# Kernel optimization log

Hardware: AMD Instinct MI355X
Metric: run time of the kernel (lower is better)

Reference implementation:

```python
import jax, jax.numpy as jnp
import numpy as np

B, T, D = 2, 1024, 1024
NUM_HEADS_ARG = 16
HS = D // NUM_HEADS_ARG          # 64 (per-head size)
H = HS                           # bug in source: num_heads passed = head_size -> 64 heads
FF = 4 * D
EPS = 1e-5


def _layernorm(x, gamma, beta):
    mu = jnp.mean(x, axis=-1, keepdims=True)
    var = jnp.mean(jnp.square(x - mu), axis=-1, keepdims=True)
    return (x - mu) * jax.lax.rsqrt(var + EPS) * gamma + beta


def setup_inputs() -> dict:
    key = jax.random.key(0)
    ks = jax.random.split(key, 12)
    s_d = 1.0 / np.sqrt(D)
    s_cat = 1.0 / np.sqrt(H * HS)
    s_ff = 1.0 / np.sqrt(FF)
    return {
        "x": jax.random.normal(ks[0], (B, T, D), jnp.float32),
        "Wq": jax.random.uniform(ks[1], (H, D, HS), jnp.float32, -s_d, s_d),
        "Wk": jax.random.uniform(ks[2], (H, D, HS), jnp.float32, -s_d, s_d),
        "Wv": jax.random.uniform(ks[3], (H, D, HS), jnp.float32, -s_d, s_d),
        "Wo": jax.random.uniform(ks[4], (H * HS, D), jnp.float32, -s_cat, s_cat),
        "bo": jax.random.uniform(ks[5], (D,), jnp.float32, -s_cat, s_cat),
        "W1": jax.random.uniform(ks[6], (D, FF), jnp.float32, -s_d, s_d),
        "b1": jax.random.uniform(ks[7], (FF,), jnp.float32, -s_d, s_d),
        "W2": jax.random.uniform(ks[8], (FF, D), jnp.float32, -s_ff, s_ff),
        "b2": jax.random.uniform(ks[9], (D,), jnp.float32, -s_ff, s_ff),
        "g1": jnp.ones((D,), jnp.float32),
        "be1": jnp.zeros((D,), jnp.float32),
        "g2": jnp.ones((D,), jnp.float32),
        "be2": jnp.zeros((D,), jnp.float32),
    }


def reference(x, Wq, Wk, Wv, Wo, bo, W1, b1, W2, b2, g1, be1, g2, be2):
    # per-head projections (no bias): [B,H,T,hs]
    q = jnp.einsum('btd,hde->bhte', x, Wq)
    k = jnp.einsum('btd,hde->bhte', x, Wk)
    v = jnp.einsum('btd,hde->bhte', x, Wv)
    scores = jnp.einsum('bhte,bhse->bhts', q, k) / np.sqrt(HS)  # [B,H,T,T]
    causal = jnp.tril(jnp.ones((T, T), bool))
    scores = jnp.where(causal, scores, -jnp.inf)
    probs = jax.nn.softmax(scores, axis=-1)
    att = jnp.einsum('bhts,bhse->bhte', probs, v)               # [B,H,T,hs]
    # torch stack(dim=3) -> [B,T,hs,H] then flatten: index = d*H + h
    cat = jnp.transpose(att, (0, 2, 3, 1)).reshape(B, T, HS * H)
    mha = cat @ Wo + bo
    x1 = _layernorm(x + mha, g1, be1)
    ff = jax.nn.relu(x1 @ W1 + b1) @ W2 + b2
    return _layernorm(x1 + ff, g2, be2)
```

## Files before the change

### kernel.cpp

```cpp
#include <hip/hip_runtime.h>

typedef unsigned short u16;
typedef __bf16 bf16x8 __attribute__((ext_vector_type(8)));
typedef float f32x4 __attribute__((ext_vector_type(4)));

#define B_ 2
#define T_ 1024
#define D_ 1024
#define H_ 64
#define HS_ 64
#define FF_ 4096
#define SZ_QKV 8388608L
#define S_SCALE 0.1803368801111f

__device__ __forceinline__ float bf2f(u16 u) {
  union { unsigned int v; float f; } x; x.v = ((unsigned int)u) << 16; return x.f;
}
__device__ __forceinline__ u16 f2bf(float f) {
  union { float f; unsigned int v; } x; x.f = f;
  unsigned int r = x.v + 0x7fffu + ((x.v >> 16) & 1u);
  return (u16)(r >> 16);
}
__device__ __forceinline__ u16 f2bf_rtz(float f) {
  union { float f; unsigned int v; } x; x.f = f;
  return (u16)(x.v >> 16);
}

typedef __attribute__((address_space(3))) unsigned int lds_u32;
typedef __attribute__((address_space(1))) const unsigned int glb_u32;
__device__ __forceinline__ void gload_lds16(const void* g, void* l) {
  __builtin_amdgcn_global_load_lds((glb_u32*)g, (lds_u32*)l, 16, 0, 0);
}

__global__ __launch_bounds__(256) void prep(
    const float* __restrict__ x, const float* __restrict__ Wq,
    const float* __restrict__ Wk, const float* __restrict__ Wv,
    const float* __restrict__ Wo, const float* __restrict__ W1,
    const float* __restrict__ W2,
    u16* __restrict__ xb, u16* __restrict__ Wqkvt, u16* __restrict__ Wot,
    u16* __restrict__ W1t, u16* __restrict__ W2t)
{
  __shared__ float tile[64][65];
  int id = blockIdx.x;
  if (id < 1024) {
    const long i = ((long)id * 256 + threadIdx.x) * 8;
    float4 a = *(const float4*)(x + i);
    float4 b = *(const float4*)(x + i + 4);
    union { uint4 v; u16 u[8]; } o;
    o.u[0]=f2bf(a.x); o.u[1]=f2bf(a.y); o.u[2]=f2bf(a.z); o.u[3]=f2bf(a.w);
    o.u[4]=f2bf(b.x); o.u[5]=f2bf(b.y); o.u[6]=f2bf(b.z); o.u[7]=f2bf(b.w);
    *(uint4*)(xb + i) = o.v;
    return;
  }
  id -= 1024;
  const float* in; u16* out; long ibase, obase; int in_rs, out_rs, r0, c0;
  if (id < 3072) {
    const int w = id >> 10, rem = id & 1023;
    const int z = rem >> 4, rt = rem & 15;
    in = (w == 0) ? Wq : (w == 1) ? Wk : Wv;
    ibase = (long)z * 65536; in_rs = 64; r0 = rt * 64; c0 = 0;
    out = Wqkvt + (long)w * 4194304;
    obase = (long)z * 65536; out_rs = 1024;
  } else if (id < 4096) {
    const int rem = id - 3072;
    const int z = rem >> 4, ct = rem & 15;
    in = Wo; ibase = (long)z * 1024; in_rs = 65536; r0 = 0; c0 = ct * 64;
    out = Wot; obase = (long)z * 64; out_rs = 4096;
  } else if (id < 5120) {
    const int rem = id - 4096;
    const int rt = rem >> 6, ct = rem & 63;
    in = W1; ibase = 0; in_rs = 4096; r0 = rt * 64; c0 = ct * 64;
    out = W1t; obase = 0; out_rs = 1024;
  } else {
    const int rem = id - 5120;
    const int rt = rem >> 4, ct = rem & 15;
    in = W2; ibase = 0; in_rs = 1024; r0 = rt * 64; c0 = ct * 64;
    out = W2t; obase = 0; out_rs = 4096;
  }
  const int t = threadIdx.x, lr = t >> 4, lc4 = (t & 15) * 4;
  #pragma unroll
  for (int j = 0; j < 4; ++j) {
    float4 f = *(const float4*)(in + ibase + (long)(r0 + lr + j * 16) * in_rs + c0 + lc4);
    tile[lr + j * 16][lc4]     = f.x;
    tile[lr + j * 16][lc4 + 1] = f.y;
    tile[lr + j * 16][lc4 + 2] = f.z;
    tile[lr + j * 16][lc4 + 3] = f.w;
  }
  __syncthreads();
  const int cr = t >> 3, ch = t & 7;
  #pragma unroll
  for (int j2 = 0; j2 < 2; ++j2) {
    const int crr = cr + j2 * 32;
    union { uint4 v; u16 u[8]; } o;
    #pragma unroll
    for (int i = 0; i < 8; ++i) o.u[i] = f2bf(tile[ch * 8 + i][crr]);
    *(uint4*)(out + obase + (long)(c0 + crr) * out_rs + r0 + ch * 8) = o.v;
  }
}

template<int EPI, int LDA, int LDB>
__global__ __launch_bounds__(512, 2) void gemm8b(
    const u16* __restrict__ A, const u16* __restrict__ Bt, u16* __restrict__ C,
    const float* __restrict__ bias, int K, int koff, int ldc)
{
  __shared__ __attribute__((aligned(16))) u16 As[3][256 * 64];
  __shared__ __attribute__((aligned(16))) u16 Bs[3][128 * 64];
  const int nwg = gridDim.x, cpx = nwg >> 3;
  const int sid = (blockIdx.x & 7) * cpx + (blockIdx.x >> 3);
  const int bm = sid & 7, bn = sid >> 3;
  const int bz = blockIdx.z;
  const long ko = (long)bz * koff;
  const int tid = threadIdx.x, wave = tid >> 6, lane = tid & 63;
  const int quad = lane >> 4, l16 = lane & 15;
  const int wm = (wave >> 1) * 64;
  const int wn = (wave & 1) * 64;
  const int slog = ((tid & 7) ^ ((tid >> 3) & 7)) * 8;
  const int srow = tid >> 3;
  const int ph0 = ((quad)     ^ (l16 & 7)) * 8;
  const int ph1 = ((4 + quad) ^ (l16 & 7)) * 8;

  const u16* Ag = A + (long)(bm * 256) * LDA + ko + slog;
  const u16* Bg = Bt + (long)(bn * 128) * LDB + ko + slog;

  f32x4 acc[4][4];
  #pragma unroll
  for (int i = 0; i < 4; ++i)
    #pragma unroll
    for (int j = 0; j < 4; ++j) acc[i][j] = (f32x4){0.f, 0.f, 0.f, 0.f};

  const int nK = K >> 6;

  auto STAGE_A = [&](int d, int t, int a) {
    gload_lds16(Ag + (long)(a * 64 + srow) * LDA + (t << 6),
                (u16*)As[d] + a * 4096 + tid * 8);
  };
  auto STAGE_B = [&](int d, int t, int b) {
    gload_lds16(Bg + (long)(b * 64 + srow) * LDB + (t << 6),
                (u16*)Bs[d] + b * 4096 + tid * 8);
  };

  #pragma unroll
  for (int a = 0; a < 4; ++a) STAGE_A(0, 0, a);
  STAGE_B(0, 0, 0); STAGE_B(0, 0, 1);
  #pragma unroll
  for (int a = 0; a < 4; ++a) STAGE_A(1, 1, a);
  STAGE_B(1, 1, 0); STAGE_B(1, 1, 1);

  bf16x8 af[4][2], bf[4][2];
  int cur = 0;
  for (int t = 0; t < nK; ++t) {
    const int nxt = (cur >= 1) ? cur - 1 : cur + 2;
    const bool st = (t + 2) < nK;
    const u16* Ab = As[cur];
    const u16* Bb = Bs[cur];

    if (t < nK - 1) { asm volatile("s_waitcnt vmcnt(6)" ::: "memory"); }
    else            { asm volatile("s_waitcnt vmcnt(0)" ::: "memory"); }
    __builtin_amdgcn_sched_barrier(0);
    __builtin_amdgcn_s_barrier();
    __builtin_amdgcn_sched_barrier(0);

    #pragma unroll
    for (int ii = 0; ii < 2; ++ii) {
      const u16* r = Ab + (wm + ii * 16 + l16) * 64;
      af[ii][0] = *(const bf16x8*)(r + ph0);
      af[ii][1] = *(const bf16x8*)(r + ph1);
    }
    #pragma unroll
    for (int jj = 0; jj < 2; ++jj) {
      const u16* r = Bb + (wn + jj * 16 + l16) * 64;
      bf[jj][0] = *(const bf16x8*)(r + ph0);
      bf[jj][1] = *(const bf16x8*)(r + ph1);
    }
    if (st) { STAGE_A(nxt, t + 2, 0); STAGE_A(nxt, t + 2, 1); }
    __builtin_amdgcn_sched_barrier(0);
    __builtin_amdgcn_s_setprio(1);
    #pragma unroll
    for (int ii = 0; ii < 2; ++ii)
      #pragma unroll
      for (int jj = 0; jj < 2; ++jj) {
        acc[ii][jj] = __builtin_amdgcn_mfma_f32_16x16x32_bf16(af[ii][0], bf[jj][0], acc[ii][jj], 0, 0, 0);
        acc[ii][jj] = __builtin_amdgcn_mfma_f32_16x16x32_bf16(af[ii][1], bf[jj][1], acc[ii][jj], 0, 0, 0);
      }
    __builtin_amdgcn_s_setprio(0);
    __builtin_amdgcn_sched_barrier(0);

    #pragma unroll
    for (int jj = 0; jj < 2; ++jj) {
      const u16* r = Bb + (wn + (2 + jj) * 16 + l16) * 64;
      bf[2 + jj][0] = *(const bf16x8*)(r + ph0);
      bf[2 + jj][1] = *(const bf16x8*)(r + ph1);
    }
    if (st) { STAGE_A(nxt, t + 2, 2); STAGE_A(nxt, t + 2, 3); }
    __builtin_amdgcn_sched_barrier(0);
    __builtin_amdgcn_s_setprio(1);
    #pragma unroll
    for (int ii = 0; ii < 2; ++ii)
      #pragma unroll
      for (int jj = 0; jj < 2; ++jj) {
        acc[ii][2 + jj] = __builtin_amdgcn_mfma_f32_16x16x32_bf16(af[ii][0], bf[2 + jj][0], acc[ii][2 + jj], 0, 0, 0);
        acc[ii][2 + jj] = __builtin_amdgcn_mfma_f32_16x16x32_bf16(af[ii][1], bf[2 + jj][1], acc[ii][2 + jj], 0, 0, 0);
      }
    __builtin_amdgcn_s_setprio(0);
    __builtin_amdgcn_sched_barrier(0);

    #pragma unroll
    for (int ii = 0; ii < 2; ++ii) {
      const u16* r = Ab + (wm + (2 + ii) * 16 + l16) * 64;
      af[2 + ii][0] = *(const bf16x8*)(r + ph0);
      af[2 + ii][1] = *(const bf16x8*)(r + ph1);
    }
    if (st) { STAGE_B(nxt, t + 2, 0); STAGE_B(nxt, t + 2, 1); }
    __builtin_amdgcn_sched_barrier(0);
    __builtin_amdgcn_s_setprio(1);
    #pragma unroll
    for (int ii = 0; ii < 2; ++ii)
      #pragma unroll
      for (int jj = 0; jj < 2; ++jj) {
        acc[2 + ii][jj] = __builtin_amdgcn_mfma_f32_16x16x32_bf16(af[2 + ii][0], bf[jj][0], acc[2 + ii][jj], 0, 0, 0);
        acc[2 + ii][jj] = __builtin_amdgcn_mfma_f32_16x16x32_bf16(af[2 + ii][1], bf[jj][1], acc[2 + ii][jj], 0, 0, 0);
      }
    __builtin_amdgcn_s_setprio(0);
    __builtin_amdgcn_sched_barrier(0);

    __builtin_amdgcn_s_setprio(1);
    #pragma unroll
    for (int ii = 0; ii < 2; ++ii)
      #pragma unroll
      for (int jj = 0; jj < 2; ++jj) {
        acc[2 + ii][2 + jj] = __builtin_amdgcn_mfma_f32_16x16x32_bf16(af[2 + ii][0], bf[2 + jj][0], acc[2 + ii][2 + jj], 0, 0, 0);
        acc[2 + ii][2 + jj] = __builtin_amdgcn_mfma_f32_16x16x32_bf16(af[2 + ii][1], bf[2 + jj][1], acc[2 + ii][2 + jj], 0, 0, 0);
      }
    __builtin_amdgcn_s_setprio(0);

    cur = nxt == 0 ? (cur == 2 ? 0 : cur + 1) : (cur == 2 ? 0 : cur + 1);
  }

  #pragma unroll
  for (int j = 0; j < 4; ++j) {
    const int col = bn * 128 + wn + j * 16 + l16;
    const float bval = (EPI == 1) ? bias[col] : 0.f;
    #pragma unroll
    for (int i = 0; i < 4; ++i) {
      #pragma unroll
      for (int r = 0; r < 4; ++r) {
        const int row = bm * 256 + wm + i * 16 + quad * 4 + r;
        float vv = acc[i][j][r] + bval;
        if (EPI == 1) vv = fmaxf(vv, 0.f);
        if (EPI == 2) {
          const int which = col >> 12, rem = col & 4095;
          const int h = rem >> 6, e = rem & 63;
          const int bb = row >> 10, tt = row & 1023;
          C[(long)which * SZ_QKV + ((long)((bb << 6) + h)) * 65536L + tt * 64 + e] = f2bf(vv);
        } else if (EPI == 3) {
          ((float*)C)[(long)bz * 2097152 + (long)row * ldc + col] = vv;
        } else {
          C[(long)row * ldc + col] = f2bf(vv);
        }
      }
    }
  }
}

__global__ __launch_bounds__(256) void attn_flash(
    const u16* __restrict__ Q, const u16* __restrict__ Kg,
    const u16* __restrict__ V, u16* __restrict__ Om)
{
  __shared__ __attribute__((aligned(16))) u16 Ks[2][64][72];
  __shared__ __attribute__((aligned(16))) u16 Vs[2][64][72];
  __shared__ __attribute__((aligned(16))) u16 QP[4][16][72];
  const int bh = blockIdx.x;
  const int qt = gridDim.y - 1 - blockIdx.y;
  const int b = bh >> 6, h = bh & 63;
  const long base = (long)bh * (T_ * HS_);
  const int tid = threadIdx.x;
  const int wave = tid >> 6, lane = tid & 63, quad = lane >> 4, l16 = lane & 15;
  const int sm = tid >> 2, sc = (tid & 3) * 16;
  const int vswz = (sc >> 4) << 3;

  {
    const int qr = lane >> 3, qe = (lane & 7) * 8;
    #pragma unroll
    for (int j = 0; j < 2; ++j) {
      union { uint4 v; u16 u[8]; } a, o;
      a.v = *(const uint4*)(Q + base + (long)(qt * 64 + wave * 16 + qr + j * 8) * HS_ + qe);
      #pragma unroll
      for (int i = 0; i < 8; ++i) o.u[i] = f2bf(bf2f(a.u[i]) * S_SCALE);
      *(uint4*)&QP[wave][qr + j * 8][qe] = o.v;
    }
  }
  bf16x8 aq0 = *(const bf16x8*)&QP[wave][l16][quad * 8];
  bf16x8 aq1 = *(const bf16x8*)&QP[wave][l16][32 + quad * 8];

  float psum[4] = { 0.f, 0.f, 0.f, 0.f };
  f32x4 oacc[4] = { {0,0,0,0}, {0,0,0,0}, {0,0,0,0}, {0,0,0,0} };

  uint4 kA, kB, vA, vB;
  kA = *(const uint4*)(Kg + base + (long)sm * HS_ + sc);
  kB = *(const uint4*)(Kg + base + (long)sm * HS_ + sc + 8);
  vA = *(const uint4*)(V  + base + (long)sm * HS_ + sc);
  vB = *(const uint4*)(V  + base + (long)sm * HS_ + sc + 8);
  {
    *(uint4*)&Ks[0][sm][sc] = kA; *(uint4*)&Ks[0][sm][sc + 8] = kB;
    union { uint4 v; u16 u[8]; } t0, t1; t0.v = vA; t1.v = vB;
    #pragma unroll
    for (int i = 0; i < 8; ++i) Vs[0][sc + i][sm ^ vswz] = t0.u[i];
    #pragma unroll
    for (int i = 0; i < 8; ++i) Vs[0][sc + 8 + i][sm ^ vswz] = t1.u[i];
  }
  __syncthreads();

  for (int kt = 0; kt <= qt; ++kt) {
    const int cur = kt & 1;
    const bool pf = (kt < qt);
    if (pf) {
      const long nb = base + (long)((kt + 1) * 64 + sm) * HS_ + sc;
      kA = *(const uint4*)(Kg + nb); kB = *(const uint4*)(Kg + nb + 8);
      vA = *(const uint4*)(V  + nb); vB = *(const uint4*)(V  + nb + 8);
    }

    f32x4 sacc[4] = { {0,0,0,0}, {0,0,0,0}, {0,0,0,0}, {0,0,0,0} };
    #pragma unroll
    for (int nt = 0; nt < 4; ++nt) {
      bf16x8 b0 = *(const bf16x8*)&Ks[cur][nt * 16 + l16][quad * 8];
      bf16x8 b1 = *(const bf16x8*)&Ks[cur][nt * 16 + l16][32 + quad * 8];
      sacc[nt] = __builtin_amdgcn_mfma_f32_16x16x32_bf16(aq0, b0, sacc[nt], 0, 0, 0);
      sacc[nt] = __builtin_amdgcn_mfma_f32_16x16x32_bf16(aq1, b1, sacc[nt], 0, 0, 0);
    }

    if (kt == qt) {
      #pragma unroll
      for (int nt = 0; nt < 4; ++nt) {
        const int col = nt * 16 + l16;
        #pragma unroll
        for (int r = 0; r < 4; ++r) {
          const int row = wave * 16 + quad * 4 + r;
          float p = exp2f(sacc[nt][r]);
          p = (col <= row) ? p : 0.f;
          sacc[nt][r] = p; psum[r] += p;
        }
      }
    } else {
      #pragma unroll
      for (int nt = 0; nt < 4; ++nt)
        #pragma unroll
        for (int r = 0; r < 4; ++r) {
          const float p = exp2f(sacc[nt][r]);
          sacc[nt][r] = p; psum[r] += p;
        }
    }

    #pragma unroll
    for (int nt = 0; nt < 4; ++nt)
      #pragma unroll
      for (int r = 0; r < 4; ++r)
        QP[wave][quad * 4 + r][nt * 16 + l16] = f2bf_rtz(sacc[nt][r]);
    bf16x8 p0 = *(const bf16x8*)&QP[wave][l16][quad * 8];
    bf16x8 p1 = *(const bf16x8*)&QP[wave][l16][32 + quad * 8];

    #pragma unroll
    for (int et = 0; et < 4; ++et) {
      const int c0 = ((quad ^ et) * 8);
      bf16x8 b0 = *(const bf16x8*)&Vs[cur][et * 16 + l16][c0];
      bf16x8 b1 = *(const bf16x8*)&Vs[cur][et * 16 + l16][32 + c0];
      oacc[et] = __builtin_amdgcn_mfma_f32_16x16x32_bf16(p0, b0, oacc[et], 0, 0, 0);
      oacc[et] = __builtin_amdgcn_mfma_f32_16x16x32_bf16(p1, b1, oacc[et], 0, 0, 0);
    }

    if (pf) {
      const int nxt = 1 - cur;
      *(uint4*)&Ks[nxt][sm][sc] = kA; *(uint4*)&Ks[nxt][sm][sc + 8] = kB;
      union { uint4 v; u16 u[8]; } t0, t1; t0.v = vA; t1.v = vB;
      #pragma unroll
      for (int i = 0; i < 8; ++i) Vs[nxt][sc + i][sm ^ vswz] = t0.u[i];
      #pragma unroll
      for (int i = 0; i < 8; ++i) Vs[nxt][sc + 8 + i][sm ^ vswz] = t1.u[i];
    }
    __syncthreads();
  }

  #pragma unroll
  for (int off = 1; off < 16; off <<= 1)
    #pragma unroll
    for (int r = 0; r < 4; ++r)
      psum[r] += __shfl_xor(psum[r], off, 64);
  u16 (*Os)[72] = Ks[0];
  #pragma unroll
  for (int r = 0; r < 4; ++r) {
    const float rinv = 1.f / fmaxf(psum[r], 1e-20f);
    const int row = wave * 16 + quad * 4 + r;
    #pragma unroll
    for (int et = 0; et < 4; ++et)
      Os[row][et * 16 + l16] = f2bf(oacc[et][r] * rinv);
  }
  const int orow = wave * 16 + (lane >> 3), oe = (lane & 7) * 8;
  #pragma unroll
  for (int it = 0; it < 2; ++it) {
    const int rr = orow + it * 8;
    uint4 o = *(const uint4*)&Os[rr][oe];
    *(uint4*)(Om + ((long)(b * T_ + qt * 64 + rr)) * 4096 + h * 64 + oe) = o;
  }
}

template<int XBF, int OBF>
__global__ __launch_bounds__(256) void ln_sum4(
    const float* __restrict__ P4, const float* __restrict__ bias,
    const void* __restrict__ Xv, const float* __restrict__ g,
    const float* __restrict__ be, void* __restrict__ outv)
{
  __shared__ float red[8];
  const int row = blockIdx.x, tid = threadIdx.x;
  const long base = (long)row * D_;
  float v4[4]; float s = 0.f;
  #pragma unroll
  for (int j = 0; j < 4; ++j) {
    const int i = tid + j * 256;
    float acc = bias[i];
    #pragma unroll
    for (int p = 0; p < 4; ++p) acc += P4[(long)p * 2097152 + base + i];
    const float xval = XBF ? bf2f(((const u16*)Xv)[base + i]) : ((const float*)Xv)[base + i];
    v4[j] = xval + acc;
    s += v4[j];
  }
  #pragma unroll
  for (int off = 32; off > 0; off >>= 1) s += __shfl_down(s, off, 64);
  if ((tid & 63) == 0) red[tid >> 6] = s;
  __syncthreads();
  const float mu = (red[0] + red[1] + red[2] + red[3]) * (1.f / D_);
  float vs = 0.f;
  #pragma unroll
  for (int j = 0; j < 4; ++j) { const float d = v4[j] - mu; vs += d * d; }
  #pragma unroll
  for (int off = 32; off > 0; off >>= 1) vs += __shfl_down(vs, off, 64);
  __syncthreads();
  if ((tid & 63) == 0) red[tid >> 6] = vs;
  __syncthreads();
  const float rs = rsqrtf((red[0] + red[1] + red[2] + red[3]) * (1.f / D_) + 1e-5f);
  #pragma unroll
  for (int j = 0; j < 4; ++j) {
    const int i = tid + j * 256;
    const float o = (v4[j] - mu) * rs * g[i] + be[i];
    if (OBF) ((u16*)outv)[base + i] = f2bf(o);
    else     ((float*)outv)[base + i] = o;
  }
}

extern "C" void kernel_launch(void* const* d_in, const int* in_sizes, int n_in,
                              void* d_out, int out_size, void* d_ws, size_t ws_size,
                              hipStream_t stream) {
  const float* x   = (const float*)d_in[0];
  const float* Wq  = (const float*)d_in[1];
  const float* Wk  = (const float*)d_in[2];
  const float* Wv  = (const float*)d_in[3];
  const float* Wo  = (const float*)d_in[4];
  const float* bo  = (const float*)d_in[5];
  const float* W1  = (const float*)d_in[6];
  const float* b1  = (const float*)d_in[7];
  const float* W2  = (const float*)d_in[8];
  const float* b2  = (const float*)d_in[9];
  const float* g1  = (const float*)d_in[10];
  const float* be1 = (const float*)d_in[11];
  const float* g2  = (const float*)d_in[12];
  const float* be2 = (const float*)d_in[13];
  float* out = (float*)d_out;

  u16* ws = (u16*)d_ws;
  u16* xb    = ws;
  u16* Wqkvt = xb + 2097152;
  u16* Wot   = Wqkvt + 12582912;
  u16* W1t   = Wot + 4194304;
  u16* W2t   = W1t + 4194304;
  u16* q     = W2t + 4194304;
  u16* k     = q + SZ_QKV;
  u16* v     = k + SZ_QKV;
  u16* Om    = v + SZ_QKV;
  float* P1 = (float*)q;
  float* P2 = (float*)q;
  u16* x1  = v;
  u16* h1  = Om;

  dim3 blk(256);
  dim3 blk8(512);

  prep<<<dim3(7168), blk, 0, stream>>>(x, Wq, Wk, Wv, Wo, W1, W2,
                                       xb, Wqkvt, Wot, W1t, W2t);

  gemm8b<2, 1024, 1024><<<dim3(768), blk8, 0, stream>>>(
      xb, Wqkvt, q, nullptr, 1024, 0, 0);

  attn_flash<<<dim3(128, 16), blk, 0, stream>>>(q, k, v, Om);

  gemm8b<3, 4096, 4096><<<dim3(64, 1, 4), blk8, 0, stream>>>(
      Om, Wot, (u16*)P1, nullptr, 1024, 1024, 1024);

  ln_sum4<0, 1><<<dim3(2048), blk, 0, stream>>>(P1, bo, x, g1, be1, x1);

  gemm8b<1, 1024, 1024><<<dim3(256), blk8, 0, stream>>>(
      x1, W1t, h1, b1, 1024, 0, 4096);

  gemm8b<3, 4096, 4096><<<dim3(64, 1, 4), blk8, 0, stream>>>(
      h1, W2t, (u16*)P2, nullptr, 1024, 1024, 1024);

  ln_sum4<1, 0><<<dim3(2048), blk, 0, stream>>>(P2, b2, x1, g2, be2, out);

  (void)in_sizes; (void)n_in; (void)out_size; (void)ws_size;
}
```

Baseline: 357.5 us.

## Switch GEMM to 4-wave blocks with K=32 steps and larger per-wave tiles

Replaces the 8-wave 256x128 GEMM with a 4-wave version. Each wave now computes a 128x64 sub-tile with 8x4 accumulators, and the K step per stage drops from 64 to 32, with a new LDS layout and swizzle that packs two rows per 64-element line. Fewer waves mean less barrier overhead, more register-level reuse of A/B fragments, and half the LDS footprint per block. The cost is higher accumulator register pressure, which may limit occupancy, plus twice as many loop iterations and barriers per K.

```diff
diff --git a/kernel.cpp b/kernel.cpp
--- a/kernel.cpp
+++ b/kernel.cpp
@@ -99,12 +99,12 @@
 }
 
 template<int EPI, int LDA, int LDB>
-__global__ __launch_bounds__(512, 2) void gemm8b(
+__global__ __launch_bounds__(256, 2) void gemm4w(
     const u16* __restrict__ A, const u16* __restrict__ Bt, u16* __restrict__ C,
     const float* __restrict__ bias, int K, int koff, int ldc)
 {
-  __shared__ __attribute__((aligned(16))) u16 As[3][256 * 64];
-  __shared__ __attribute__((aligned(16))) u16 Bs[3][128 * 64];
+  __shared__ __attribute__((aligned(16))) u16 As[3][8192];
+  __shared__ __attribute__((aligned(16))) u16 Bs[3][4096];
   const int nwg = gridDim.x, cpx = nwg >> 3;
   const int sid = (blockIdx.x & 7) * cpx + (blockIdx.x >> 3);
   const int bm = sid & 7, bn = sid >> 3;
@@ -112,31 +112,33 @@
   const long ko = (long)bz * koff;
   const int tid = threadIdx.x, wave = tid >> 6, lane = tid & 63;
   const int quad = lane >> 4, l16 = lane & 15;
-  const int wm = (wave >> 1) * 64;
+  const int wm = (wave >> 1) * 128;
   const int wn = (wave & 1) * 64;
-  const int slog = ((tid & 7) ^ ((tid >> 3) & 7)) * 8;
-  const int srow = tid >> 3;
-  const int ph0 = ((quad)     ^ (l16 & 7)) * 8;
-  const int ph1 = ((4 + quad) ^ (l16 & 7)) * 8;
-
-  const u16* Ag = A + (long)(bm * 256) * LDA + ko + slog;
-  const u16* Bg = Bt + (long)(bn * 128) * LDB + ko + slog;
-
-  f32x4 acc[4][4];
-  #pragma unroll
-  for (int i = 0; i < 4; ++i)
+
+  const int u_ = (tid & 7) ^ ((tid >> 3) & 7);
+  const int srow = 2 * (tid >> 3) + (u_ >> 2);
+  const int scol = (u_ & 3) * 8;
+  const int sA = ((((l16 & 1) << 2) + quad) ^ (l16 >> 1)) * 8;
+  const int Lb = l16 >> 1;
+
+  const u16* Ag = A + (long)(bm * 256 + srow) * LDA + ko + scol;
+  const u16* Bg = Bt + (long)(bn * 128 + srow) * LDB + ko + scol;
+
+  f32x4 acc[8][4];
+  #pragma unroll
+  for (int i = 0; i < 8; ++i)
     #pragma unroll
     for (int j = 0; j < 4; ++j) acc[i][j] = (f32x4){0.f, 0.f, 0.f, 0.f};
 
-  const int nK = K >> 6;
+  const int nK = K >> 5;
 
   auto STAGE_A = [&](int d, int t, int a) {
-    gload_lds16(Ag + (long)(a * 64 + srow) * LDA + (t << 6),
-                (u16*)As[d] + a * 4096 + tid * 8);
+    gload_lds16(Ag + (long)(a * 64) * LDA + (t << 5),
+                (u16*)As[d] + a * 2048 + tid * 8);
   };
   auto STAGE_B = [&](int d, int t, int b) {
-    gload_lds16(Bg + (long)(b * 64 + srow) * LDB + (t << 6),
-                (u16*)Bs[d] + b * 4096 + tid * 8);
+    gload_lds16(Bg + (long)(b * 64) * LDB + (t << 5),
+                (u16*)Bs[d] + b * 2048 + tid * 8);
   };
 
   #pragma unroll
@@ -146,10 +148,10 @@
   for (int a = 0; a < 4; ++a) STAGE_A(1, 1, a);
   STAGE_B(1, 1, 0); STAGE_B(1, 1, 1);
 
-  bf16x8 af[4][2], bf[4][2];
+  bf16x8 af[8], bf[4];
   int cur = 0;
   for (int t = 0; t < nK; ++t) {
-    const int nxt = (cur >= 1) ? cur - 1 : cur + 2;
+    const int nxt = (cur >= 1) ? cur - 1 : 2;
     const bool st = (t + 2) < nK;
     const u16* Ab = As[cur];
     const u16* Bb = Bs[cur];
@@ -161,79 +163,59 @@
     __builtin_amdgcn_sched_barrier(0);
 
     #pragma unroll
-    for (int ii = 0; ii < 2; ++ii) {
-      const u16* r = Ab + (wm + ii * 16 + l16) * 64;
-      af[ii][0] = *(const bf16x8*)(r + ph0);
-      af[ii][1] = *(const bf16x8*)(r + ph1);
-    }
-    #pragma unroll
-    for (int jj = 0; jj < 2; ++jj) {
-      const u16* r = Bb + (wn + jj * 16 + l16) * 64;
-      bf[jj][0] = *(const bf16x8*)(r + ph0);
-      bf[jj][1] = *(const bf16x8*)(r + ph1);
-    }
+    for (int i = 0; i < 4; ++i)
+      af[i] = *(const bf16x8*)&Ab[((wm >> 1) + i * 8 + Lb) * 64 + sA];
+    #pragma unroll
+    for (int j = 0; j < 2; ++j)
+      bf[j] = *(const bf16x8*)&Bb[((wn >> 1) + j * 8 + Lb) * 64 + sA];
     if (st) { STAGE_A(nxt, t + 2, 0); STAGE_A(nxt, t + 2, 1); }
     __builtin_amdgcn_sched_barrier(0);
     __builtin_amdgcn_s_setprio(1);
     #pragma unroll
-    for (int ii = 0; ii < 2; ++ii)
-      #pragma unroll
-      for (int jj = 0; jj < 2; ++jj) {
-        acc[ii][jj] = __builtin_amdgcn_mfma_f32_16x16x32_bf16(af[ii][0], bf[jj][0], acc[ii][jj], 0, 0, 0);
-        acc[ii][jj] = __builtin_amdgcn_mfma_f32_16x16x32_bf16(af[ii][1], bf[jj][1], acc[ii][jj], 0, 0, 0);
-      }
+    for (int i = 0; i < 4; ++i)
+      #pragma unroll
+      for (int j = 0; j < 2; ++j)
+        acc[i][j] = __builtin_amdgcn_mfma_f32_16x16x32_bf16(af[i], bf[j], acc[i][j], 0, 0, 0);
     __builtin_amdgcn_s_setprio(0);
     __builtin_amdgcn_sched_barrier(0);
 
     #pragma unroll
-    for (int jj = 0; jj < 2; ++jj) {
-      const u16* r = Bb + (wn + (2 + jj) * 16 + l16) * 64;
-      bf[2 + jj][0] = *(const bf16x8*)(r + ph0);
-      bf[2 + jj][1] = *(const bf16x8*)(r + ph1);
-    }
+    for (int j = 0; j < 2; ++j)
+      bf[2 + j] = *(const bf16x8*)&Bb[((wn >> 1) + (2 + j) * 8 + Lb) * 64 + sA];
     if (st) { STAGE_A(nxt, t + 2, 2); STAGE_A(nxt, t + 2, 3); }
     __builtin_amdgcn_sched_barrier(0);
     __builtin_amdgcn_s_setprio(1);
     #pragma unroll
-    for (int ii = 0; ii < 2; ++ii)
-      #pragma unroll
-      for (int jj = 0; jj < 2; ++jj) {
-        acc[ii][2 + jj] = __builtin_amdgcn_mfma_f32_16x16x32_bf16(af[ii][0], bf[2 + jj][0], acc[ii][2 + jj], 0, 0, 0);
-        acc[ii][2 + jj] = __builtin_amdgcn_mfma_f32_16x16x32_bf16(af[ii][1], bf[2 + jj][1], acc[ii][2 + jj], 0, 0, 0);
-      }
+    for (int i = 0; i < 4; ++i)
+      #pragma unroll
+      for (int j = 0; j < 2; ++j)
+        acc[i][2 + j] = __builtin_amdgcn_mfma_f32_16x16x32_bf16(af[i], bf[2 + j], acc[i][2 + j], 0, 0, 0);
     __builtin_amdgcn_s_setprio(0);
     __builtin_amdgcn_sched_barrier(0);
 
     #pragma unroll
-    for (int ii = 0; ii < 2; ++ii) {
-      const u16* r = Ab + (wm + (2 + ii) * 16 + l16) * 64;
-      af[2 + ii][0] = *(const bf16x8*)(r + ph0);
-      af[2 + ii][1] = *(const bf16x8*)(r + ph1);
-    }
+    for (int i = 0; i < 4; ++i)
+      af[4 + i] = *(const bf16x8*)&Ab[((wm >> 1) + (4 + i) * 8 + Lb) * 64 + sA];
     if (st) { STAGE_B(nxt, t + 2, 0); STAGE_B(nxt, t + 2, 1); }
     __builtin_amdgcn_sched_barrier(0);
     __builtin_amdgcn_s_setprio(1);
     #pragma unroll
-    for (int ii = 0; ii < 2; ++ii)
-      #pragma unroll
-      for (int jj = 0; jj < 2; ++jj) {
-        acc[2 + ii][jj] = __builtin_amdgcn_mfma_f32_16x16x32_bf16(af[2 + ii][0], bf[jj][0], acc[2 + ii][jj], 0, 0, 0);
-        acc[2 + ii][jj] = __builtin_amdgcn_mfma_f32_16x16x32_bf16(af[2 + ii][1], bf[jj][1], acc[2 + ii][jj], 0, 0, 0);
-      }
+    for (int i = 0; i < 4; ++i)
+      #pragma unroll
+      for (int j = 0; j < 2; ++j)
+        acc[4 + i][j] = __builtin_amdgcn_mfma_f32_16x16x32_bf16(af[4 + i], bf[j], acc[4 + i][j], 0, 0, 0);
     __builtin_amdgcn_s_setprio(0);
     __builtin_amdgcn_sched_barrier(0);
 
     __builtin_amdgcn_s_setprio(1);
     #pragma unroll
-    for (int ii = 0; ii < 2; ++ii)
-      #pragma unroll
-      for (int jj = 0; jj < 2; ++jj) {
-        acc[2 + ii][2 + jj] = __builtin_amdgcn_mfma_f32_16x16x32_bf16(af[2 + ii][0], bf[2 + jj][0], acc[2 + ii][2 + jj], 0, 0, 0);
-        acc[2 + ii][2 + jj] = __builtin_amdgcn_mfma_f32_16x16x32_bf16(af[2 + ii][1], bf[2 + jj][1], acc[2 + ii][2 + jj], 0, 0, 0);
-      }
+    for (int i = 0; i < 4; ++i)
+      #pragma unroll
+      for (int j = 0; j < 2; ++j)
+        acc[4 + i][2 + j] = __builtin_amdgcn_mfma_f32_16x16x32_bf16(af[4 + i], bf[2 + j], acc[4 + i][2 + j], 0, 0, 0);
     __builtin_amdgcn_s_setprio(0);
 
-    cur = nxt == 0 ? (cur == 2 ? 0 : cur + 1) : (cur == 2 ? 0 : cur + 1);
+    cur = (cur == 2) ? 0 : cur + 1;
   }
 
   #pragma unroll
@@ -241,7 +223,7 @@
     const int col = bn * 128 + wn + j * 16 + l16;
     const float bval = (EPI == 1) ? bias[col] : 0.f;
     #pragma unroll
-    for (int i = 0; i < 4; ++i) {
+    for (int i = 0; i < 8; ++i) {
       #pragma unroll
       for (int r = 0; r < 4; ++r) {
         const int row = bm * 256 + wm + i * 16 + quad * 4 + r;
@@ -480,25 +462,24 @@
   u16* h1  = Om;
 
   dim3 blk(256);
-  dim3 blk8(512);
 
   prep<<<dim3(7168), blk, 0, stream>>>(x, Wq, Wk, Wv, Wo, W1, W2,
                                        xb, Wqkvt, Wot, W1t, W2t);
 
-  gemm8b<2, 1024, 1024><<<dim3(768), blk8, 0, stream>>>(
+  gemm4w<2, 1024, 1024><<<dim3(768), blk, 0, stream>>>(
       xb, Wqkvt, q, nullptr, 1024, 0, 0);
 
   attn_flash<<<dim3(128, 16), blk, 0, stream>>>(q, k, v, Om);
 
-  gemm8b<3, 4096, 4096><<<dim3(64, 1, 4), blk8, 0, stream>>>(
+  gemm4w<3, 4096, 4096><<<dim3(64, 1, 4), blk, 0, stream>>>(
       Om, Wot, (u16*)P1, nullptr, 1024, 1024, 1024);
 
   ln_sum4<0, 1><<<dim3(2048), blk, 0, stream>>>(P1, bo, x, g1, be1, x1);
 
-  gemm8b<1, 1024, 1024><<<dim3(256), blk8, 0, stream>>>(
+  gemm4w<1, 1024, 1024><<<dim3(256), blk, 0, stream>>>(
       x1, W1t, h1, b1, 1024, 0, 4096);
 
-  gemm8b<3, 4096, 4096><<<dim3(64, 1, 4), blk8, 0, stream>>>(
+  gemm4w<3, 4096, 4096><<<dim3(64, 1, 4), blk, 0, stream>>>(
       h1, W2t, (u16*)P2, nullptr, 1024, 1024, 1024);
 
   ln_sum4<1, 0><<<dim3(2048), blk, 0, stream>>>(P2, b2, x1, g2, be2, out);
```

After: 393.6 us. 1.1x slower.
